# Kernel optimization log

Measured on AMD Instinct MI355X. Metric: run time of the kernel, lower is better.

The kernel has to match this reference:

```python
import jax, jax.numpy as jnp
import numpy as np

B, S, V, D, G, H, L, K = 32, 256, 100000, 128, 128, 256, 32, 3
ALPHA = 0.5


def lstm_pass(x, mask, W, U, b, reverse):
    # x: (B,S,I), mask: (B,S) bool. PyTorch gate order i,f,g,o.
    Bh = x.shape[0]
    Hd = U.shape[0]
    h0 = jnp.zeros((Bh, Hd), x.dtype)
    c0 = jnp.zeros((Bh, Hd), x.dtype)

    def step(carry, inp):
        h, c = carry
        xt, mt = inp
        g = xt @ W + h @ U + b
        i, f, gg, o = jnp.split(g, 4, axis=-1)
        i = jax.nn.sigmoid(i)
        f = jax.nn.sigmoid(f)
        gg = jnp.tanh(gg)
        o = jax.nn.sigmoid(o)
        cn = f * c + i * gg
        hn = o * jnp.tanh(cn)
        m = mt[:, None]
        h = jnp.where(m, hn, h)
        c = jnp.where(m, cn, c)
        return (h, c), h * m.astype(h.dtype)

    _, hs = jax.lax.scan(step, (h0, c0), (x.transpose(1, 0, 2), mask.T), reverse=reverse)
    return hs.transpose(1, 0, 2)  # (B,S,Hd), zero at padded steps (like pad_packed)


def setup_inputs() -> dict:
    key = jax.random.key(0)
    ks = jax.random.split(key, 24)
    word_inputs = jax.random.randint(ks[0], (B, S), 0, V)
    lens = jnp.sort(jax.random.randint(ks[1], (B,), S // 2, S + 1))[::-1]
    mask = (jnp.arange(S)[None, :] < lens[:, None])
    idx_inputs = jax.random.randint(ks[2], (B, S), 0, V)
    char_inputs = jax.random.randint(ks[3], (B * S, 4), 0, 100)
    char_seq_lengths = jnp.ones((B * S,), jnp.int64 if jax.config.jax_enable_x64 else jnp.int32)
    char_seq_recover = jnp.arange(B * S)
    s = lambda k, sh, sc: jax.random.normal(k, sh, jnp.float32) * sc
    I = D + G
    inp = {
        'word_inputs': word_inputs,
        'word_seq_lengths': lens,
        'char_inputs': char_inputs,
        'char_seq_lengths': char_seq_lengths,
        'char_seq_recover': char_seq_recover,
        'mask': mask,
        'idx_inputs': idx_inputs,
        'word_embedding': s(ks[4], (V, D), 0.1),
        'label_embedding': s(ks[5], (L, D), 0.1),
        'sent_W': s(ks[6], (D, G), 1.0 / np.sqrt(D)),
        'sent_b': jnp.zeros((G,), jnp.float32),
        'conv_W': s(ks[7], (L, L, K), 1.0 / np.sqrt(L * K)),
        'conv_b': jnp.zeros((L,), jnp.float32),
        'lstm_Wf': s(ks[8], (I, 4 * H // 2), 1.0 / np.sqrt(I)),
        'lstm_Uf': s(ks[9], (H // 2, 4 * H // 2), 1.0 / np.sqrt(H // 2)),
        'lstm_bf': jnp.zeros((4 * H // 2,), jnp.float32),
        'lstm_Wb': s(ks[10], (I, 4 * H // 2), 1.0 / np.sqrt(I)),
        'lstm_Ub': s(ks[11], (H // 2, 4 * H // 2), 1.0 / np.sqrt(H // 2)),
        'lstm_bb': jnp.zeros((4 * H // 2,), jnp.float32),
        'tag_W': s(ks[12], (H, L), 1.0 / np.sqrt(H)),
        'tag_b': jnp.zeros((L,), jnp.float32),
        'mem_W': s(ks[13], (H, L), 1.0 / np.sqrt(H)),
        'mem_b': jnp.zeros((L,), jnp.float32),
        'mem_bank': s(ks[14], (V, H), 0.1),
    }
    return inp


def reference(word_inputs, word_seq_lengths, char_inputs, char_seq_lengths, char_seq_recover,
              mask, idx_inputs, word_embedding, label_embedding, sent_W, sent_b,
              conv_W, conv_b, lstm_Wf, lstm_Uf, lstm_bf, lstm_Wb, lstm_Ub, lstm_bb,
              tag_W, tag_b, mem_W, mem_b, mem_bank):
    maskf = mask.astype(jnp.float32)
    # ---- WordRep: embeddings + label cosine similarity ----
    we = word_embedding[word_inputs]  # (B,S,D) gather
    wn = we / (jnp.linalg.norm(we, axis=-1, keepdims=True) + 1e-8)
    ln = label_embedding / (jnp.linalg.norm(label_embedding, axis=-1, keepdims=True) + 1e-8)
    label_embs = jnp.einsum('bsd,ld->bsl', wn, ln)  # (B,S,L)
    # ---- SentenceRep (projection stand-in) + label attention pooling ----
    sent_hidden = jnp.tanh(we @ sent_W + sent_b)  # (B,S,G)
    lf = jax.lax.conv_general_dilated(
        label_embs.transpose(0, 2, 1), conv_W, (1,), [(K // 2, K // 2)],
        dimension_numbers=('NCH', 'OIH', 'NCH')) + conv_b[None, :, None]
    lf = jax.nn.relu(lf).transpose(0, 2, 1)  # (B,S,L)
    lm = lf.max(axis=-1)  # (B,S)
    # partial (masked) softmax, exactly as in the torch code
    e = jnp.exp(lm) * maskf
    attn = e / e.sum(axis=1, keepdims=True)
    sent_rep = jnp.einsum('bs,bsg->bg', attn, sent_hidden)[:, None, :]  # bmm
    sent_rep = jnp.broadcast_to(sent_rep, (B, S, G))  # repeat over seq
    # ---- BiLSTM over concat(word, sentence) ----
    wr = jnp.concatenate([we, sent_rep], axis=-1)  # (B,S,D+G)
    hf = lstm_pass(wr, mask, lstm_Wf, lstm_Uf, lstm_bf, False)
    hb = lstm_pass(wr, mask, lstm_Wb, lstm_Ub, lstm_bb, True)
    feat = jnp.concatenate([hf, hb], axis=-1)  # (B,S,H)
    outputs = feat @ tag_W + tag_b  # (B,S,L)
    # ---- MemoryBank: gather keyed by word id, zero padded positions ----
    doc_h = mem_bank[word_inputs] * maskf[..., None]  # (B,S,H) irregular gather
    doc_rep = doc_h @ mem_W + mem_b  # mem2tag
    # bank update (side effect in torch; computed functionally, not returned)
    new_bank = mem_bank.at[idx_inputs.reshape(-1)].set(
        (feat * maskf[..., None]).reshape(-1, H))
    del new_bank
    return outputs * (1.0 - ALPHA) + doc_rep * ALPHA
```

## Files before the change

kernel.cpp:

```cpp
#include <hip/hip_runtime.h>
#include <hip/hip_bf16.h>

#define BB 32
#define SS 256
#define DD 128
#define GG 128
#define NG 512
#define LL 32
#define LOG2E 1.4426950408889634f

typedef unsigned short u16;
typedef __attribute__((ext_vector_type(8))) short short8;
typedef __attribute__((ext_vector_type(4))) float f32x4;

__device__ __forceinline__ float bf2f(u16 u){ return __uint_as_float(((unsigned)u)<<16); }
__device__ __forceinline__ u16 f2bf(float f){
    unsigned x = __float_as_uint(f);
    unsigned r = x + 0x7fffu + ((x>>16)&1u);
    return (u16)(r>>16);
}
__device__ __forceinline__ float tanh_f(float x){ float e=__expf(2.0f*x); return 1.0f - 2.0f/(e+1.0f); }

__device__ __forceinline__ float exp2_f(float x){
#if __has_builtin(__builtin_amdgcn_exp2f)
    return __builtin_amdgcn_exp2f(x);
#elif __has_builtin(__builtin_amdgcn_expf)
    return __builtin_amdgcn_expf(x);
#else
    return __expf(x * 0.6931471805599453f);
#endif
}
__device__ __forceinline__ float rcp_f(float x){
#if __has_builtin(__builtin_amdgcn_rcpf)
    return __builtin_amdgcn_rcpf(x);
#else
    return 1.0f / x;
#endif
}

#define NJOBS 22
struct PJobs { const void* src[NJOBS]; int n[NJOBS]; int p0[NJOBS]; int p1[NJOBS];
               int type[NJOBS]; int blk0[NJOBS]; };

__global__ void kprep(PJobs jb, const void* __restrict__ wemb, const int* __restrict__ wid,
                      int* __restrict__ flags, float* __restrict__ can,
                      u16* __restrict__ WcatT, u16* __restrict__ tagWT, u16* __restrict__ memWT,
                      u16* __restrict__ weC, float* __restrict__ invn){
    int t = threadIdx.x;
    __shared__ int cw[4];
    __shared__ int sflag;
    {
        u16 v = ((const u16*)wemb)[2*t];
        int e = (v>>7)&0xFF;
        int c = (e>=0x90)?1:0;
        #pragma unroll
        for (int mk=32; mk>0; mk>>=1) c += __shfl_xor(c, mk);
        if ((t&63)==0) cw[t>>6] = c;
        __syncthreads();
        if (t==0) sflag = (cw[0]+cw[1]+cw[2]+cw[3] >= 32) ? 1 : 0;
        __syncthreads();
    }
    int f = sflag;
    if (blockIdx.x==0 && t==0) flags[0] = f;

    int bx = blockIdx.x;
    int id = 0;
    #pragma unroll
    for (int jj=1; jj<NJOBS; jj++) if (bx >= jb.blk0[jj]) id = jj;
    int i = (bx - jb.blk0[id])*256 + t;
    if (i >= jb.n[id]) return;
    const void* src = jb.src[id];
    int p0 = jb.p0[id];
    int ty = jb.type[id];
    if (ty == 0){
        float v = f ? ((const float*)src)[i] : bf2f(((const u16*)src)[i]);
        can[p0 + i] = v;
    } else if (ty == 1){
        int c = i>>7, k = i&127;
        float v = f ? ((const float*)src)[k*jb.p1[id] + c] : bf2f(((const u16*)src)[k*jb.p1[id] + c]);
        WcatT[(size_t)(p0 + c)*128 + k] = f2bf(v);
    } else if (ty == 2){
        int l = i&31, k = i>>5;
        float v = f ? ((const float*)src)[k*32 + l] : bf2f(((const u16*)src)[k*32 + l]);
        (p0 ? memWT : tagWT)[l*256 + k] = f2bf(v);
    } else if (ty == 3){
        int row = i>>7, col = i&127;
        float v = f ? ((const float*)src)[i] : bf2f(((const u16*)src)[i]);
        float sq = v*v;
        #pragma unroll
        for (int mk=32; mk>0; mk>>=1) sq += __shfl_xor(sq, mk);
        __shared__ float r4[4];
        if ((t&63)==0) r4[t>>6] = sq;
        __syncthreads();
        int half = t>>7;
        float tot = r4[half*2] + r4[half*2+1];
        float inv = 1.0f/(sqrtf(tot) + 1e-8f);
        WcatT[(size_t)(1152+row)*128 + col] = f2bf(v*inv);
        WcatT[(size_t)(1184+row)*128 + col] = 0;
    } else if (ty == 4){
        int c = i>>7, k = i&127;
        float v = f ? ((const float*)src)[k*512 + c] : bf2f(((const u16*)src)[k*512 + c]);
        int q = c>>7, rem = c&127, w5 = rem>>4, li = rem&15;
        WcatT[(size_t)(p0 + w5*64 + q*16 + li)*128 + k] = f2bf(v);
    } else {
        int tok = i>>5, lane = i&31;
        int idx = wid[tok];
        float v0,v1,v2,v3;
        if (f){
            f32x4 u = *(const f32x4*)((const float*)wemb + (size_t)idx*DD + lane*4);
            v0=u[0]; v1=u[1]; v2=u[2]; v3=u[3];
        } else {
            ushort4 u = *(const ushort4*)((const u16*)wemb + (size_t)idx*DD + lane*4);
            v0=bf2f(u.x); v1=bf2f(u.y); v2=bf2f(u.z); v3=bf2f(u.w);
        }
        int b = tok>>8, s = tok&255;
        int m = s*BB + b;
        ushort4 wv;
        wv.x=f2bf(v0); wv.y=f2bf(v1); wv.z=f2bf(v2); wv.w=f2bf(v3);
        *(ushort4*)&weC[(size_t)m*DD + lane*4] = wv;
        float sq = v0*v0 + v1*v1 + v2*v2 + v3*v3;
        #pragma unroll
        for (int mk=16; mk>0; mk>>=1) sq += __shfl_xor(sq, mk);
        if (lane==0) invn[m] = 1.0f/(sqrtf(sq) + 1e-8f);
    }
}

__global__ __launch_bounds__(256) void kgemm(const u16* __restrict__ weC,
                      const u16* __restrict__ WcatT,
                      const float* __restrict__ invn, const float* __restrict__ sentBc,
                      float* __restrict__ gpre4, float* __restrict__ sent_h,
                      float* __restrict__ lab_e){
    int mt = blockIdx.x;
    int nb = blockIdx.y;
    int t = threadIdx.x;
    int w4 = t>>6, l = t&63, li = l&15, lg = l>>4;
    int mbase = mt*64 + w4*16;
    int n0 = nb*64;
    short8 af[4];
    #pragma unroll
    for (int ks=0;ks<4;ks++)
        af[ks] = *(const short8*)&weC[(size_t)(mbase + li)*128 + ks*32 + lg*8];
    f32x4 acc[4];
    #pragma unroll
    for (int nt=0;nt<4;nt++){
        short8 bf[4];
        #pragma unroll
        for (int ks=0;ks<4;ks++)
            bf[ks] = *(const short8*)&WcatT[(size_t)(n0 + nt*16 + li)*128 + ks*32 + lg*8];
        f32x4 a; a[0]=0.f; a[1]=0.f; a[2]=0.f; a[3]=0.f;
        #pragma unroll
        for (int ks=0;ks<4;ks++)
            a = __builtin_amdgcn_mfma_f32_16x16x32_bf16(af[ks], bf[ks], a, 0,0,0);
        acc[nt] = a;
    }
    if (nb < 16){
        int dir = nb>>3, w5 = nb&7;
        int s = mt*2 + (w4>>1);
        int bg = (w4&1)*4 + lg;
        float* gp = gpre4 + ((((size_t)(dir*8+bg)*256 + s)*8 + w5)*256);
        #pragma unroll
        for (int r=0;r<4;r++){
            f32x4 v;
            v[0] = acc[0][r]*LOG2E;
            v[1] = acc[1][r]*LOG2E;
            v[2] = acc[2][r]*(2.0f*LOG2E);
            v[3] = acc[3][r]*LOG2E;
            *(f32x4*)&gp[(r*16 + li)*4] = v;
        }
    } else {
        int mrow = mbase + lg*4;
        #pragma unroll
        for (int nt=0;nt<4;nt++){
            int n = n0 + nt*16 + li;
            if (n < 1152){
                int c = n - 1024;
                float bb = sentBc[c];
                #pragma unroll
                for (int r=0;r<4;r++){
                    int m = mrow + r;
                    int b = m&31, s = m>>5;
                    sent_h[((size_t)(b*256+s))*128 + c] = tanh_f(acc[nt][r] + bb);
                }
            } else if (n < 1184){
                int c = n - 1152;
                #pragma unroll
                for (int r=0;r<4;r++){
                    int m = mrow + r;
                    int b = m&31, s = m>>5;
                    lab_e[((size_t)(b*256+s))*32 + c] = acc[nt][r] * invn[m];
                }
            }
        }
    }
}

__global__ __launch_bounds__(256) void k23p(const float* __restrict__ lab_e,
                        const float* __restrict__ convWc, const float* __restrict__ convBc,
                        const float* __restrict__ sent_h,
                        const int* __restrict__ lens,
                        float* __restrict__ srp, float* __restrict__ esum_p){
    int b = blockIdx.x, stile = blockIdx.y, t = threadIdx.x;
    int sl = t>>3, oq = t&7;
    int s = stile*32 + sl;
    __shared__ float le_s[34*33];
    __shared__ float wle[LL*LL*3];
    __shared__ float wb[LL];
    __shared__ float es[32];
    __shared__ float red[2][GG];
    int s0 = stile*32;
    for (int i=t; i<34*32; i+=256){
        int row = i>>5, col = i&31;
        int sg = s0 - 1 + row;
        le_s[row*33 + col] = (sg>=0 && sg<SS) ? lab_e[(size_t)b*SS*LL + sg*LL + col] : 0.f;
    }
    for (int i=t; i<LL*LL*3; i+=256) wle[i] = convWc[i];
    if (t < LL) wb[t] = convBc[t];
    __syncthreads();
    float lm = 0.f;
    #pragma unroll
    for (int op=0; op<4; op++){
        int o = oq*4 + op;
        float a0 = wb[o], a1 = 0.f, a2 = 0.f;
        #pragma unroll
        for (int i=0;i<LL;i++){
            a0 = fmaf(le_s[(sl+0)*33+i], wle[o*96 + i*3    ], a0);
            a1 = fmaf(le_s[(sl+1)*33+i], wle[o*96 + i*3 + 1], a1);
            a2 = fmaf(le_s[(sl+2)*33+i], wle[o*96 + i*3 + 2], a2);
        }
        lm = fmaxf(lm, fmaxf(a0+a1+a2, 0.f));
    }
    #pragma unroll
    for (int mk=1; mk<8; mk<<=1) lm = fmaxf(lm, __shfl_xor(lm, mk));
    if (oq == 0) es[sl] = (s < lens[b]) ? __expf(lm) : 0.f;
    __syncthreads();
    int col = t&127, sh = t>>7;
    float a0 = 0.f, a1 = 0.f;
    int sb = s0 + sh*16;
    #pragma unroll
    for (int s2=0; s2<16; s2+=2){
        a0 = fmaf(es[sh*16+s2],   sent_h[((size_t)b*SS + sb+s2)*GG + col], a0);
        a1 = fmaf(es[sh*16+s2+1], sent_h[((size_t)b*SS + sb+s2+1)*GG + col], a1);
    }
    red[sh][col] = a0+a1;
    __syncthreads();
    if (t < GG) srp[((size_t)b*8 + stile)*GG + t] = red[0][t] + red[1][t];
    if (t < 32){
        float e = es[t];
        #pragma unroll
        for (int mk=16; mk>0; mk>>=1) e += __shfl_xor(e, mk);
        if (t==0) esum_p[b*8 + stile] = e;
    }
}

__global__ void k3b_cpart(const float* __restrict__ srp, const float* __restrict__ esum_p,
                          const float* __restrict__ Wfc, const float* __restrict__ Wbc,
                          const float* __restrict__ bfc, const float* __restrict__ bbc,
                          float* __restrict__ cpart){
    int chunk = blockIdx.x, b = blockIdx.y, t = threadIdx.x;
    __shared__ float srs[GG];
    if (t < GG){
        float a = 0.f;
        #pragma unroll
        for (int st=0; st<8; st++) a += srp[((size_t)b*8 + st)*GG + t];
        float es = 0.f;
        #pragma unroll
        for (int st=0; st<8; st++) es += esum_p[b*8 + st];
        srs[t] = a * (1.0f/es);
    }
    __syncthreads();
    int ng = chunk*256 + t;
    int dir = ng>>9, n = ng&511;
    const float* W = dir ? Wbc : Wfc;
    float c0 = (dir ? bbc : bfc)[n], c1 = 0.f;
    for (int g=0; g<GG; g+=2){
        c0 = fmaf(srs[g],   W[(size_t)(DD+g)*NG + n], c0);
        c1 = fmaf(srs[g+1], W[(size_t)(DD+g+1)*NG + n], c1);
    }
    cpart[((size_t)dir*NG + n)*BB + b] = c0+c1;
}

__global__ __launch_bounds__(512) void k5_lstm(const float* __restrict__ gpre4,
                       const float* __restrict__ Ufc, const float* __restrict__ Ubc,
                       const float* __restrict__ cpart,
                       const int* __restrict__ lens, float* __restrict__ feat){
    int dir = blockIdx.x>>3, bg = blockIdx.x&7;
    int t = threadIdx.x;
    int w = t>>6, l = t&63, lg = l>>4, li = l&15;
    int j = w*16 + li;
    int b = bg*4 + lg;
    const float* Uc = dir ? Ubc : Ufc;

    short8 bfr[4][4];
    #pragma unroll
    for (int q=0;q<4;q++){
        float sc = (q==2) ? 2.0f*LOG2E : LOG2E;
        #pragma unroll
        for (int ks=0;ks<4;ks++){
            int n = q*128 + j;
            short8 v;
            #pragma unroll
            for (int jj=0;jj<8;jj++)
                v[jj] = (short)f2bf(Uc[(size_t)(ks*32 + lg*8 + jj)*NG + n] * sc);
            bfr[q][ks] = v;
        }
    }
    float cpr[4];
    #pragma unroll
    for (int q=0;q<4;q++)
        cpr[q] = cpart[((size_t)(dir*NG + q*128 + j))*BB + b] * ((q==2) ? 2.0f*LOG2E : LOG2E);
    int len1 = lens[b];

    __shared__ u16 Hhi[2][16*128];
    for (int i=t; i<2*2048; i+=512) ((u16*)Hhi)[i] = 0;

    bool rdp = ((li & 3) == 0);
    int roff[4];
    #pragma unroll
    for (int ks=0;ks<4;ks++)
        roff[ks] = (li*256 + ((ks*64 + lg*16) ^ ((li&7)<<4))) >> 1;
    int woff;
    { int row = lg*4; woff = (row*256 + ((2*j) ^ ((row&7)<<4))) >> 1; }

    short8 ah[4];
    #pragma unroll
    for (int ks=0;ks<4;ks++){
        #pragma unroll
        for (int jj=0;jj<8;jj++) ah[ks][jj] = 0;
    }
    f32x4 acv[4];
    #pragma unroll
    for (int q=0;q<4;q++){ acv[q][0]=0.f; acv[q][1]=0.f; acv[q][2]=0.f; acv[q][3]=0.f; }

    float c = 0.f, h = 0.f;
    int sgn = dir ? -1 : 1;
    int s0 = dir ? (SS-1) : 0;
    const float* gl = gpre4 + ((size_t)(dir*8 + bg)*256 + s0)*2048 + w*256 + l*4;
    ptrdiff_t gstep = (ptrdiff_t)sgn * 2048;

    f32x4 gA = *(const f32x4*)gl;
    f32x4 gB = *(const f32x4*)(gl + gstep);
    const float* glp = gl + 2*gstep;

    float* fb = feat + ((size_t)b*SS + s0)*256 + dir*128 + j;
    ptrdiff_t fstep = (ptrdiff_t)sgn * 256;

    int s = s0;
    __syncthreads();

#define K5_STEP(P, G)                                                          \
    {                                                                          \
        if (rdp){                                                              \
            ah[0] = *(const short8*)&Hhi[P][roff[0]];                          \
            ah[1] = *(const short8*)&Hhi[P][roff[1]];                          \
            ah[2] = *(const short8*)&Hhi[P][roff[2]];                          \
            ah[3] = *(const short8*)&Hhi[P][roff[3]];                          \
        }                                                                      \
        acv[0][0] = G[0]+cpr[0];                                               \
        acv[1][0] = G[1]+cpr[1];                                               \
        acv[2][0] = G[2]+cpr[2];                                               \
        acv[3][0] = G[3]+cpr[3];                                               \
        if (tt2 + 2 < SS){ G = *(const f32x4*)glp; glp += gstep; }             \
        _Pragma("unroll")                                                      \
        for (int ks=0;ks<4;ks++){                                              \
            _Pragma("unroll")                                                  \
            for (int q=0;q<4;q++)                                              \
                acv[q] = __builtin_amdgcn_mfma_f32_16x16x32_bf16(ah[ks], bfr[q][ks], acv[q], 0,0,0); \
        }                                                                      \
        float si = rcp_f(1.0f + exp2_f(-acv[0][0]));                           \
        float sf = rcp_f(1.0f + exp2_f(-acv[1][0]));                           \
        float tg = 1.0f - 2.0f*rcp_f(exp2_f(acv[2][0]) + 1.0f);                \
        float so = rcp_f(1.0f + exp2_f(-acv[3][0]));                           \
        float cn = sf*c + si*tg;                                               \
        float th = 1.0f - 2.0f*rcp_f(exp2_f(cn*(2.0f*LOG2E)) + 1.0f);          \
        float hn = so*th;                                                      \
        if (s < 128){ c = cn; h = hn; fb[0] = hn; }                            \
        else { bool mm = (s < len1); c = mm?cn:c; h = mm?hn:h; fb[0] = mm?hn:0.f; } \
        Hhi[P^1][woff] = f2bf(h);                                              \
        asm volatile("s_waitcnt lgkmcnt(0)" ::: "memory");                     \
        __builtin_amdgcn_sched_barrier(0);                                     \
        __builtin_amdgcn_s_barrier();                                          \
        __builtin_amdgcn_sched_barrier(0);                                     \
        s += sgn; fb += fstep;                                                 \
    }

    for (int tt=0; tt<SS; tt+=2){
        { int tt2 = tt;   K5_STEP(0, gA) }
        { int tt2 = tt+1; K5_STEP(1, gB) }
    }
#undef K5_STEP
}

__global__ __launch_bounds__(256) void k6_final(const float* __restrict__ feat,
                         const int* __restrict__ wid,
                         const int* __restrict__ lens,
                         const u16* __restrict__ tagWT, const float* __restrict__ tagBc,
                         const u16* __restrict__ memWT, const float* __restrict__ memBc,
                         const void* __restrict__ bank, const int* __restrict__ flags,
                         void* __restrict__ out){
    int t = threadIdx.x;
    int tl = t>>5, lcol = t&31;
    int tok0 = blockIdx.x*8;
    __shared__ float fr_s[8][256];
    __shared__ float br_s[8][256];
    __shared__ int idxs[8];
    __shared__ int msks[8];
    if (t < 8){
        int tok = tok0 + t;
        idxs[t] = wid[tok];
        msks[t] = ((tok&255) < lens[tok>>8]) ? 1 : 0;
    }
    __syncthreads();
    int f32m = flags[0];
    {
        const float* fp = feat + (size_t)(tok0+tl)*256 + lcol*8;
        f32x4 u0 = *(const f32x4*)fp;
        f32x4 u1 = *(const f32x4*)(fp+4);
        *(f32x4*)&fr_s[tl][lcol*8]   = u0;
        *(f32x4*)&fr_s[tl][lcol*8+4] = u1;
    }
    if (msks[tl]){
        if (f32m){
            const float* bp = (const float*)bank + (size_t)idxs[tl]*256 + lcol*8;
            f32x4 u0 = *(const f32x4*)bp;
            f32x4 u1 = *(const f32x4*)(bp+4);
            *(f32x4*)&br_s[tl][lcol*8]   = u0;
            *(f32x4*)&br_s[tl][lcol*8+4] = u1;
        } else {
            short8 bv = *(const short8*)((const u16*)bank + (size_t)idxs[tl]*256 + lcol*8);
            #pragma unroll
            for (int e=0;e<8;e++) br_s[tl][lcol*8+e] = bf2f((u16)bv[e]);
        }
    } else {
        #pragma unroll
        for (int e=0;e<8;e++) br_s[tl][lcol*8+e] = 0.f;
    }
    __syncthreads();
    float a0 = tagBc[lcol], a1=0.f, a2=0.f, a3=0.f;
    float b0 = memBc[lcol], b1=0.f, b2=0.f, b3=0.f;
    #pragma unroll 4
    for (int cc=0; cc<32; cc++){
        short8 tw = *(const short8*)&tagWT[lcol*256 + cc*8];
        short8 mw = *(const short8*)&memWT[lcol*256 + cc*8];
        f32x4 f0 = *(const f32x4*)&fr_s[tl][cc*8];
        f32x4 f1 = *(const f32x4*)&fr_s[tl][cc*8+4];
        f32x4 g0 = *(const f32x4*)&br_s[tl][cc*8];
        f32x4 g1 = *(const f32x4*)&br_s[tl][cc*8+4];
        a0 = fmaf(f0[0], bf2f((u16)tw[0]), a0);
        a1 = fmaf(f0[1], bf2f((u16)tw[1]), a1);
        a2 = fmaf(f0[2], bf2f((u16)tw[2]), a2);
        a3 = fmaf(f0[3], bf2f((u16)tw[3]), a3);
        a0 = fmaf(f1[0], bf2f((u16)tw[4]), a0);
        a1 = fmaf(f1[1], bf2f((u16)tw[5]), a1);
        a2 = fmaf(f1[2], bf2f((u16)tw[6]), a2);
        a3 = fmaf(f1[3], bf2f((u16)tw[7]), a3);
        b0 = fmaf(g0[0], bf2f((u16)mw[0]), b0);
        b1 = fmaf(g0[1], bf2f((u16)mw[1]), b1);
        b2 = fmaf(g0[2], bf2f((u16)mw[2]), b2);
        b3 = fmaf(g0[3], bf2f((u16)mw[3]), b3);
        b0 = fmaf(g1[0], bf2f((u16)mw[4]), b0);
        b1 = fmaf(g1[1], bf2f((u16)mw[5]), b1);
        b2 = fmaf(g1[2], bf2f((u16)mw[6]), b2);
        b3 = fmaf(g1[3], bf2f((u16)mw[7]), b3);
    }
    float r1 = (a0+a1)+(a2+a3);
    float r2 = (b0+b1)+(b2+b3);
    float res = 0.5f*r1 + 0.5f*r2;
    int tok = tok0 + tl;
    if (f32m) ((float*)out)[(size_t)tok*LL + lcol] = res;
    else      ((u16*)out)[(size_t)tok*LL + lcol]   = f2bf(res);
}

extern "C" void kernel_launch(void* const* d_in, const int* in_sizes, int n_in,
                              void* d_out, int out_size, void* d_ws, size_t ws_size,
                              hipStream_t stream){
    const int* wid  = (const int*)d_in[0];
    const int* lens = (const int*)d_in[1];

    char* ws = (char*)d_ws;
    int*   flags  = (int*)  (ws + 0);
    float* can    = (float*)(ws + 1024);
    u16*   WcatT  = (u16*)  (ws + 1900544);
    u16*   tagWT  = (u16*)  (ws + 2211840);
    u16*   memWT  = (u16*)  (ws + 2228224);
    float* invn   = (float*)(ws + 2244608);
    float* cpart  = (float*)(ws + 2277376);
    float* srp    = (float*)(ws + 2441216);
    float* esum_p = (float*)(ws + 2572288);
    u16*   weC    = (u16*)  (ws + 4194304);
    float* lab_e  = (float*)(ws + 8388608);
    float* sent_h = (float*)(ws + 9437184);
    float* gpre4  = (float*)(ws + 16777216);
    float* feat   = (float*)(ws + 50331648);

    float* sentBc = can + 20480;
    float* convWc = can + 20608;
    float* convBc = can + 23680;
    float* Wfc    = can + 23712;
    float* Wbc    = can + 154784;
    float* bfc    = can + 285856;
    float* bbc    = can + 286368;
    float* Ufc    = can + 286880;
    float* Ubc    = can + 352416;
    float* tagBc  = can + 426144;
    float* memBc  = can + 434368;

    static const int cn_n[15]   = {4096,16384,128,3072,32,131072,131072,512,512,65536,65536,8192,32,8192,32};
    static const int cn_src[15] = {8,9,10,11,12,13,16,15,18,14,17,19,20,21,22};
    PJobs jb;
    int nblk = 0;
    {
        int off = 0;
        for (int i=0;i<15;i++){
            jb.src[i]=d_in[cn_src[i]]; jb.n[i]=cn_n[i]; jb.p0[i]=off; jb.p1[i]=0; jb.type[i]=0;
            off+=cn_n[i];
        }
        jb.src[15]=d_in[13]; jb.n[15]=65536;  jb.p0[15]=0;    jb.p1[15]=512; jb.type[15]=4;
        jb.src[16]=d_in[16]; jb.n[16]=65536;  jb.p0[16]=512;  jb.p1[16]=512; jb.type[16]=4;
        jb.src[17]=d_in[9];  jb.n[17]=16384;  jb.p0[17]=1024; jb.p1[17]=128; jb.type[17]=1;
        jb.src[18]=d_in[19]; jb.n[18]=8192;   jb.p0[18]=0;    jb.p1[18]=0;   jb.type[18]=2;
        jb.src[19]=d_in[21]; jb.n[19]=8192;   jb.p0[19]=1;    jb.p1[19]=0;   jb.type[19]=2;
        jb.src[20]=d_in[8];  jb.n[20]=4096;   jb.p0[20]=0;    jb.p1[20]=0;   jb.type[20]=3;
        jb.src[21]=d_in[7];  jb.n[21]=262144; jb.p0[21]=0;    jb.p1[21]=0;   jb.type[21]=5;
        for (int i=0;i<NJOBS;i++){ jb.blk0[i] = nblk; nblk += (jb.n[i] + 255)/256; }
    }

    kprep  <<<nblk, 256, 0, stream>>>(jb, d_in[7], wid, flags, can, WcatT, tagWT, memWT,
                                      weC, invn);
    kgemm  <<<dim3(128,19), 256, 0, stream>>>(weC, WcatT, invn, sentBc, gpre4, sent_h, lab_e);
    k23p   <<<dim3(32,8), 256, 0, stream>>>(lab_e, convWc, convBc, sent_h, lens, srp, esum_p);
    k3b_cpart<<<dim3(4,32), 256, 0, stream>>>(srp, esum_p, Wfc, Wbc, bfc, bbc, cpart);
    k5_lstm<<<16, 512, 0, stream>>>(gpre4, Ufc, Ubc, cpart, lens, feat);
    k6_final<<<1024, 256, 0, stream>>>(feat, wid, lens, tagWT, tagBc, memWT, memBc,
                                       d_in[23], flags, d_out);
}
```

Baseline: 207.2 us.

## Fuse label-attention and sentence-projection kernels into one per-batch kernel

Merges the conv/attention kernel and the cpart projection kernel into a single kernel with one block per batch row. That block loops over all 8 sequence tiles, reduces the softmax denominator and the weighted sentence sum in shared memory, and then computes cpart directly. This removes one kernel launch and the srp/esum_p round trip through global memory. In exchange, grid parallelism drops from 256+128 blocks to only 32, so each block does serial work on a GPU with many more compute units.

```diff
diff --git a/kernel.cpp b/kernel.cpp
--- a/kernel.cpp
+++ b/kernel.cpp
@@ -194,89 +194,86 @@
     }
 }
 
-__global__ __launch_bounds__(256) void k23p(const float* __restrict__ lab_e,
+__global__ __launch_bounds__(256) void k23f(const float* __restrict__ lab_e,
                         const float* __restrict__ convWc, const float* __restrict__ convBc,
                         const float* __restrict__ sent_h,
                         const int* __restrict__ lens,
-                        float* __restrict__ srp, float* __restrict__ esum_p){
-    int b = blockIdx.x, stile = blockIdx.y, t = threadIdx.x;
-    int sl = t>>3, oq = t&7;
-    int s = stile*32 + sl;
+                        const float* __restrict__ Wfc, const float* __restrict__ Wbc,
+                        const float* __restrict__ bfc, const float* __restrict__ bbc,
+                        float* __restrict__ cpart){
+    int b = blockIdx.x, t = threadIdx.x;
     __shared__ float le_s[34*33];
     __shared__ float wle[LL*LL*3];
     __shared__ float wb[LL];
-    __shared__ float es[32];
+    __shared__ float es_all[SS];
     __shared__ float red[2][GG];
-    int s0 = stile*32;
-    for (int i=t; i<34*32; i+=256){
-        int row = i>>5, col = i&31;
-        int sg = s0 - 1 + row;
-        le_s[row*33 + col] = (sg>=0 && sg<SS) ? lab_e[(size_t)b*SS*LL + sg*LL + col] : 0.f;
-    }
+    __shared__ float srs[GG];
+    __shared__ float ew[4];
     for (int i=t; i<LL*LL*3; i+=256) wle[i] = convWc[i];
     if (t < LL) wb[t] = convBc[t];
-    __syncthreads();
-    float lm = 0.f;
-    #pragma unroll
-    for (int op=0; op<4; op++){
-        int o = oq*4 + op;
-        float a0 = wb[o], a1 = 0.f, a2 = 0.f;
-        #pragma unroll
-        for (int i=0;i<LL;i++){
-            a0 = fmaf(le_s[(sl+0)*33+i], wle[o*96 + i*3    ], a0);
-            a1 = fmaf(le_s[(sl+1)*33+i], wle[o*96 + i*3 + 1], a1);
-            a2 = fmaf(le_s[(sl+2)*33+i], wle[o*96 + i*3 + 2], a2);
-        }
-        lm = fmaxf(lm, fmaxf(a0+a1+a2, 0.f));
-    }
-    #pragma unroll
-    for (int mk=1; mk<8; mk<<=1) lm = fmaxf(lm, __shfl_xor(lm, mk));
-    if (oq == 0) es[sl] = (s < lens[b]) ? __expf(lm) : 0.f;
-    __syncthreads();
+    int lenb = lens[b];
+    int sl = t>>3, oq = t&7;
+    for (int st=0; st<8; st++){
+        int s0 = st*32;
+        __syncthreads();
+        for (int i=t; i<34*32; i+=256){
+            int row = i>>5, col = i&31;
+            int sg = s0 - 1 + row;
+            le_s[row*33 + col] = (sg>=0 && sg<SS) ? lab_e[(size_t)b*SS*LL + sg*LL + col] : 0.f;
+        }
+        __syncthreads();
+        int s = s0 + sl;
+        float lm = 0.f;
+        #pragma unroll
+        for (int op=0; op<4; op++){
+            int o = oq*4 + op;
+            float a0 = wb[o], a1 = 0.f, a2 = 0.f;
+            #pragma unroll
+            for (int i=0;i<LL;i++){
+                a0 = fmaf(le_s[(sl+0)*33+i], wle[o*96 + i*3    ], a0);
+                a1 = fmaf(le_s[(sl+1)*33+i], wle[o*96 + i*3 + 1], a1);
+                a2 = fmaf(le_s[(sl+2)*33+i], wle[o*96 + i*3 + 2], a2);
+            }
+            lm = fmaxf(lm, fmaxf(a0+a1+a2, 0.f));
+        }
+        #pragma unroll
+        for (int mk=1; mk<8; mk<<=1) lm = fmaxf(lm, __shfl_xor(lm, mk));
+        if (oq == 0) es_all[s] = (s < lenb) ? __expf(lm) : 0.f;
+    }
+    __syncthreads();
+    {
+        float e = es_all[t];
+        #pragma unroll
+        for (int mk=32; mk>0; mk>>=1) e += __shfl_xor(e, mk);
+        if ((t&63)==0) ew[t>>6] = e;
+    }
+    __syncthreads();
+    float inv = 1.0f/(ew[0]+ew[1]+ew[2]+ew[3]);
     int col = t&127, sh = t>>7;
-    float a0 = 0.f, a1 = 0.f;
-    int sb = s0 + sh*16;
-    #pragma unroll
-    for (int s2=0; s2<16; s2+=2){
-        a0 = fmaf(es[sh*16+s2],   sent_h[((size_t)b*SS + sb+s2)*GG + col], a0);
-        a1 = fmaf(es[sh*16+s2+1], sent_h[((size_t)b*SS + sb+s2+1)*GG + col], a1);
-    }
-    red[sh][col] = a0+a1;
-    __syncthreads();
-    if (t < GG) srp[((size_t)b*8 + stile)*GG + t] = red[0][t] + red[1][t];
-    if (t < 32){
-        float e = es[t];
-        #pragma unroll
-        for (int mk=16; mk>0; mk>>=1) e += __shfl_xor(e, mk);
-        if (t==0) esum_p[b*8 + stile] = e;
-    }
-}
-
-__global__ void k3b_cpart(const float* __restrict__ srp, const float* __restrict__ esum_p,
-                          const float* __restrict__ Wfc, const float* __restrict__ Wbc,
-                          const float* __restrict__ bfc, const float* __restrict__ bbc,
-                          float* __restrict__ cpart){
-    int chunk = blockIdx.x, b = blockIdx.y, t = threadIdx.x;
-    __shared__ float srs[GG];
-    if (t < GG){
-        float a = 0.f;
-        #pragma unroll
-        for (int st=0; st<8; st++) a += srp[((size_t)b*8 + st)*GG + t];
-        float es = 0.f;
-        #pragma unroll
-        for (int st=0; st<8; st++) es += esum_p[b*8 + st];
-        srs[t] = a * (1.0f/es);
-    }
-    __syncthreads();
-    int ng = chunk*256 + t;
-    int dir = ng>>9, n = ng&511;
-    const float* W = dir ? Wbc : Wfc;
-    float c0 = (dir ? bbc : bfc)[n], c1 = 0.f;
-    for (int g=0; g<GG; g+=2){
-        c0 = fmaf(srs[g],   W[(size_t)(DD+g)*NG + n], c0);
-        c1 = fmaf(srs[g+1], W[(size_t)(DD+g+1)*NG + n], c1);
-    }
-    cpart[((size_t)dir*NG + n)*BB + b] = c0+c1;
+    {
+        float a0 = 0.f, a1 = 0.f;
+        int sb = sh*128;
+        for (int s2=sb; s2<sb+128; s2+=2){
+            a0 = fmaf(es_all[s2],   sent_h[((size_t)b*SS + s2)*GG + col], a0);
+            a1 = fmaf(es_all[s2+1], sent_h[((size_t)b*SS + s2+1)*GG + col], a1);
+        }
+        red[sh][col] = a0+a1;
+    }
+    __syncthreads();
+    if (t < GG) srs[t] = (red[0][t]+red[1][t])*inv;
+    __syncthreads();
+    #pragma unroll
+    for (int chunk=0; chunk<4; chunk++){
+        int ng = chunk*256 + t;
+        int dir = ng>>9, n = ng&511;
+        const float* W = dir ? Wbc : Wfc;
+        float c0 = (dir ? bbc : bfc)[n], c1 = 0.f;
+        for (int g=0; g<GG; g+=2){
+            c0 = fmaf(srs[g],   W[(size_t)(DD+g)*NG + n], c0);
+            c1 = fmaf(srs[g+1], W[(size_t)(DD+g+1)*NG + n], c1);
+        }
+        cpart[((size_t)dir*NG + n)*BB + b] = c0+c1;
+    }
 }
 
 __global__ __launch_bounds__(512) void k5_lstm(const float* __restrict__ gpre4,
@@ -484,8 +481,6 @@
     u16*   memWT  = (u16*)  (ws + 2228224);
     float* invn   = (float*)(ws + 2244608);
     float* cpart  = (float*)(ws + 2277376);
-    float* srp    = (float*)(ws + 2441216);
-    float* esum_p = (float*)(ws + 2572288);
     u16*   weC    = (u16*)  (ws + 4194304);
     float* lab_e  = (float*)(ws + 8388608);
     float* sent_h = (float*)(ws + 9437184);
@@ -527,8 +522,8 @@
     kprep  <<<nblk, 256, 0, stream>>>(jb, d_in[7], wid, flags, can, WcatT, tagWT, memWT,
                                       weC, invn);
     kgemm  <<<dim3(128,19), 256, 0, stream>>>(weC, WcatT, invn, sentBc, gpre4, sent_h, lab_e);
-    k23p   <<<dim3(32,8), 256, 0, stream>>>(lab_e, convWc, convBc, sent_h, lens, srp, esum_p);
-    k3b_cpart<<<dim3(4,32), 256, 0, stream>>>(srp, esum_p, Wfc, Wbc, bfc, bbc, cpart);
+    k23f   <<<32, 256, 0, stream>>>(lab_e, convWc, convBc, sent_h, lens,
+                                    Wfc, Wbc, bfc, bbc, cpart);
     k5_lstm<<<16, 512, 0, stream>>>(gpre4, Ufc, Ubc, cpart, lens, feat);
     k6_final<<<1024, 256, 0, stream>>>(feat, wid, lens, tagWT, tagBc, memWT, memBc,
                                        d_in[23], flags, d_out);
```

Result: slower. 354.0 us (+70.9%).
